# Optimization experiments

Hardware: AMD Instinct MI355X
Metric: run time of the kernel (lower is better)

Reference implementation:

```python
import jax, jax.numpy as jnp
import numpy as np

N_NODES = 500_000
N_EDGES = 5_000_000


def setup_inputs() -> dict:
    key = jax.random.key(0)
    k_x, k_e, k_w1, k_w2 = jax.random.split(key, 4)
    x = jax.random.normal(k_x, (N_NODES, 1), dtype=jnp.float32)
    edge_index = jax.random.randint(k_e, (2, N_EDGES), 0, N_NODES, dtype=jnp.int32)
    # Glorot-style init, matching PyG GCNConv default scale
    W1 = jax.random.normal(k_w1, (1, 16), dtype=jnp.float32) * np.sqrt(2.0 / (1 + 16))
    b1 = jnp.zeros((16,), dtype=jnp.float32)
    W2 = jax.random.normal(k_w2, (16, 1), dtype=jnp.float32) * np.sqrt(2.0 / (16 + 1))
    b2 = jnp.zeros((1,), dtype=jnp.float32)
    return {"x": x, "W1": W1, "b1": b1, "W2": W2, "b2": b2,
            "edge_index": edge_index}


def reference(x, W1, b1, W2, b2, edge_index):
    n = x.shape[0]
    src, dst = edge_index[0], edge_index[1]
    self_idx = jnp.arange(n, dtype=src.dtype)
    # GCNConv default: add self-loops, symmetric normalization deg^-1/2
    src_f = jnp.concatenate([src, self_idx])  # [E+N]
    dst_f = jnp.concatenate([dst, self_idx])  # [E+N]
    deg = jax.ops.segment_sum(jnp.ones(src_f.shape[0], x.dtype), dst_f,
                              num_segments=n)  # [N]
    dinv = jnp.where(deg > 0, jax.lax.rsqrt(jnp.maximum(deg, 1.0)), 0.0)
    norm = dinv[src_f] * dinv[dst_f]  # [E+N] edge weights

    def gcn_conv(h, W, b):
        h = h @ W  # [N, out]
        msg = h[src_f] * norm[:, None]  # gather + scale, [E+N, out]
        agg = jax.ops.segment_sum(msg, dst_f, num_segments=n)  # scatter-add
        return agg + b

    h = jax.nn.relu(gcn_conv(x, W1, b1))  # [N, 16]
    out = gcn_conv(h, W2, b2)  # [N, 1]
    return out.squeeze(-1)  # [N]
```

## Files before the change

### kernel.cpp

```cpp
#include <hip/hip_runtime.h>

#define N_NODES 500000
#define N_EDGES 5000000
#define NB_C 489
#define PB 512
#define EPB 9768
#define SRC_MASK 0xFFFFFu


__global__ __launch_bounds__(1024)
void hist_kernel(const int* __restrict__ dst, unsigned* __restrict__ hist) {
    __shared__ unsigned h[NB_C];
    for (int i = threadIdx.x; i < NB_C; i += 1024) h[i] = 0u;
    __syncthreads();
    const int b = blockIdx.x;
    const long s0 = (long)b * EPB;
    const int n = (int)min((long)EPB, (long)N_EDGES - s0);
    const int4* d4 = (const int4*)(dst + s0);
    const int n4 = n >> 2;
    for (int i = threadIdx.x; i < n4; i += 1024) {
        int4 d = d4[i];
        atomicAdd(&h[d.x >> 10], 1u);
        atomicAdd(&h[d.y >> 10], 1u);
        atomicAdd(&h[d.z >> 10], 1u);
        atomicAdd(&h[d.w >> 10], 1u);
    }
    __syncthreads();
    unsigned* row = hist + (size_t)b * NB_C;
    for (int i = threadIdx.x; i < NB_C; i += 1024) row[i] = h[i];
}

__global__ __launch_bounds__(512)
void prefix_kernel(unsigned* __restrict__ hist, unsigned* __restrict__ binTotal) {
    __shared__ unsigned A[PB], B[PB];
    const int bin = blockIdx.x;
    const int t = threadIdx.x;
    const unsigned c = hist[(size_t)t * NB_C + bin];
    A[t] = c;
    __syncthreads();
    unsigned* cur = A; unsigned* nxt = B;
    for (int off = 1; off < PB; off <<= 1) {
        nxt[t] = cur[t] + (t >= off ? cur[t - off] : 0u);
        __syncthreads();
        unsigned* tmp = cur; cur = nxt; nxt = tmp;
    }
    hist[(size_t)t * NB_C + bin] = cur[t] - c;
    if (t == PB - 1) binTotal[bin] = cur[PB - 1];
}

__global__ __launch_bounds__(512)
void binscan_kernel(const unsigned* __restrict__ binTotal,
                    unsigned* __restrict__ binStart) {
    __shared__ unsigned A[512], B[512];
    const int t = threadIdx.x;
    A[t] = (t < NB_C) ? binTotal[t] : 0u;
    __syncthreads();
    unsigned* cur = A; unsigned* nxt = B;
    for (int off = 1; off < 512; off <<= 1) {
        nxt[t] = cur[t] + (t >= off ? cur[t - off] : 0u);
        __syncthreads();
        unsigned* tmp = cur; cur = nxt; nxt = tmp;
    }
    if (t < NB_C) binStart[t] = (t == 0) ? 0u : cur[t - 1];
    if (t == 0) binStart[NB_C] = cur[NB_C - 1];
}

__global__ __launch_bounds__(1024)
void place_kernel(const int* __restrict__ src, const int* __restrict__ dst,
                  const unsigned* __restrict__ hist,
                  const unsigned* __restrict__ binStart,
                  unsigned* __restrict__ edgebuf) {
    __shared__ unsigned base[NB_C];
    const int b = blockIdx.x;
    const unsigned* row = hist + (size_t)b * NB_C;
    for (int i = threadIdx.x; i < NB_C; i += 1024) base[i] = binStart[i] + row[i];
    __syncthreads();
    const long s0 = (long)b * EPB;
    const int n = (int)min((long)EPB, (long)N_EDGES - s0);
    const int4* s4 = (const int4*)(src + s0);
    const int4* d4 = (const int4*)(dst + s0);
    const int n4 = n >> 2;
    for (int i = threadIdx.x; i < n4; i += 1024) {
        int4 s = s4[i];
        int4 d = d4[i];
        unsigned p;
        p = atomicAdd(&base[d.x >> 10], 1u);
        edgebuf[p] = ((unsigned)(d.x & 1023) << 20) | (unsigned)s.x;
        p = atomicAdd(&base[d.y >> 10], 1u);
        edgebuf[p] = ((unsigned)(d.y & 1023) << 20) | (unsigned)s.y;
        p = atomicAdd(&base[d.z >> 10], 1u);
        edgebuf[p] = ((unsigned)(d.z & 1023) << 20) | (unsigned)s.z;
        p = atomicAdd(&base[d.w >> 10], 1u);
        edgebuf[p] = ((unsigned)(d.w & 1023) << 20) | (unsigned)s.w;
    }
}

__global__ __launch_bounds__(1024)
void deg_dinv_kernel(const unsigned* __restrict__ edgebuf,
                     const unsigned* __restrict__ binStart,
                     const float* __restrict__ x,
                     float* __restrict__ dinv, float* __restrict__ u) {
    __shared__ unsigned cnt[1024];
    cnt[threadIdx.x] = 0u;
    __syncthreads();
    const int bin = blockIdx.x;
    const unsigned e0 = binStart[bin], e1 = binStart[bin + 1];
    const unsigned ea = (e0 + 3u) & ~3u;
    const unsigned eb = e1 & ~3u;
    for (unsigned e = e0 + threadIdx.x; e < min(ea, e1); e += 1024)
        atomicAdd(&cnt[edgebuf[e] >> 20], 1u);
    if (ea < eb) {
        const uint4* p4 = (const uint4*)(edgebuf + ea);
        const unsigned nv = (eb - ea) >> 2;
        for (unsigned i = threadIdx.x; i < nv; i += 1024) {
            uint4 r = p4[i];
            atomicAdd(&cnt[r.x >> 20], 1u);
            atomicAdd(&cnt[r.y >> 20], 1u);
            atomicAdd(&cnt[r.z >> 20], 1u);
            atomicAdd(&cnt[r.w >> 20], 1u);
        }
    }
    for (unsigned e = max(eb, min(ea, e1)) + threadIdx.x; e < e1; e += 1024)
        atomicAdd(&cnt[edgebuf[e] >> 20], 1u);
    __syncthreads();
    const int node = (bin << 10) + threadIdx.x;
    if (node < N_NODES) {
        float di = rsqrtf((float)cnt[threadIdx.x] + 1.0f);
        dinv[node] = di;
        u[node] = x[node] * di;
    }
}

__global__ __launch_bounds__(1024)
void agg1_kernel(const unsigned* __restrict__ edgebuf,
                 const unsigned* __restrict__ binStart,
                 const float* __restrict__ dinv, const float* __restrict__ u,
                 const float* __restrict__ W1, const float* __restrict__ b1,
                 const float* __restrict__ W2, float* __restrict__ w) {
    __shared__ float sum[1024];
    sum[threadIdx.x] = 0.0f;
    __syncthreads();
    const int bin = blockIdx.x;
    const unsigned e0 = binStart[bin], e1 = binStart[bin + 1];
    const unsigned ea = (e0 + 3u) & ~3u;
    const unsigned eb = e1 & ~3u;
    for (unsigned e = e0 + threadIdx.x; e < min(ea, e1); e += 1024) {
        unsigned rec = edgebuf[e];
        atomicAdd(&sum[rec >> 20], u[rec & SRC_MASK]);
    }
    if (ea < eb) {
        const uint4* p4 = (const uint4*)(edgebuf + ea);
        const unsigned nv = (eb - ea) >> 2;
        for (unsigned i = threadIdx.x; i < nv; i += 1024) {
            uint4 r = p4[i];
            atomicAdd(&sum[r.x >> 20], u[r.x & SRC_MASK]);
            atomicAdd(&sum[r.y >> 20], u[r.y & SRC_MASK]);
            atomicAdd(&sum[r.z >> 20], u[r.z & SRC_MASK]);
            atomicAdd(&sum[r.w >> 20], u[r.w & SRC_MASK]);
        }
    }
    for (unsigned e = max(eb, min(ea, e1)) + threadIdx.x; e < e1; e += 1024) {
        unsigned rec = edgebuf[e];
        atomicAdd(&sum[rec >> 20], u[rec & SRC_MASK]);
    }
    __syncthreads();
    const int node = (bin << 10) + threadIdx.x;
    if (node < N_NODES) {
        float di = dinv[node];
        float s = di * (sum[threadIdx.x] + u[node]);
        float t = 0.0f;
#pragma unroll
        for (int j = 0; j < 16; ++j) {
            float h = fmaf(W1[j], s, b1[j]);
            h = fmaxf(h, 0.0f);
            t = fmaf(h, W2[j], t);
        }
        w[node] = t * di;
    }
}

__global__ __launch_bounds__(1024)
void agg2_kernel(const unsigned* __restrict__ edgebuf,
                 const unsigned* __restrict__ binStart,
                 const float* __restrict__ dinv, const float* __restrict__ w,
                 const float* __restrict__ b2, float* __restrict__ out) {
    __shared__ float sum[1024];
    sum[threadIdx.x] = 0.0f;
    __syncthreads();
    const int bin = blockIdx.x;
    const unsigned e0 = binStart[bin], e1 = binStart[bin + 1];
    const unsigned ea = (e0 + 3u) & ~3u;
    const unsigned eb = e1 & ~3u;
    for (unsigned e = e0 + threadIdx.x; e < min(ea, e1); e += 1024) {
        unsigned rec = edgebuf[e];
        atomicAdd(&sum[rec >> 20], w[rec & SRC_MASK]);
    }
    if (ea < eb) {
        const uint4* p4 = (const uint4*)(edgebuf + ea);
        const unsigned nv = (eb - ea) >> 2;
        for (unsigned i = threadIdx.x; i < nv; i += 1024) {
            uint4 r = p4[i];
            atomicAdd(&sum[r.x >> 20], w[r.x & SRC_MASK]);
            atomicAdd(&sum[r.y >> 20], w[r.y & SRC_MASK]);
            atomicAdd(&sum[r.z >> 20], w[r.z & SRC_MASK]);
            atomicAdd(&sum[r.w >> 20], w[r.w & SRC_MASK]);
        }
    }
    for (unsigned e = max(eb, min(ea, e1)) + threadIdx.x; e < e1; e += 1024) {
        unsigned rec = edgebuf[e];
        atomicAdd(&sum[rec >> 20], w[rec & SRC_MASK]);
    }
    __syncthreads();
    const int node = (bin << 10) + threadIdx.x;
    if (node < N_NODES)
        out[node] = fmaf(dinv[node], sum[threadIdx.x] + w[node], b2[0]);
}

__global__ __launch_bounds__(256)
void deg_kernel(const int* __restrict__ dst, float* __restrict__ deg) {
    const int tid = blockIdx.x * blockDim.x + threadIdx.x;
    const int stride = gridDim.x * blockDim.x;
    const int nvec = N_EDGES / 4;
    const int4* dst4 = (const int4*)dst;
    for (int i = tid; i < nvec; i += stride) {
        int4 d = dst4[i];
        atomicAdd(&deg[d.x], 1.0f);
        atomicAdd(&deg[d.y], 1.0f);
        atomicAdd(&deg[d.z], 1.0f);
        atomicAdd(&deg[d.w], 1.0f);
    }
}
__global__ __launch_bounds__(256)
void node1_kernel(const float* __restrict__ x, float* __restrict__ deg_to_dinv,
                  float* __restrict__ u) {
    const int i = blockIdx.x * blockDim.x + threadIdx.x;
    if (i >= N_NODES) return;
    float di = rsqrtf(deg_to_dinv[i] + 1.0f);
    deg_to_dinv[i] = di;
    u[i] = x[i] * di;
}
__global__ __launch_bounds__(256)
void scatter_kernel(const int* __restrict__ src, const int* __restrict__ dst,
                    const float* __restrict__ val, float* __restrict__ acc) {
    const int tid = blockIdx.x * blockDim.x + threadIdx.x;
    const int stride = gridDim.x * blockDim.x;
    const int nvec = N_EDGES / 4;
    const int4* src4 = (const int4*)src;
    const int4* dst4 = (const int4*)dst;
    for (int i = tid; i < nvec; i += stride) {
        int4 s = src4[i];
        int4 d = dst4[i];
        atomicAdd(&acc[d.x], val[s.x]);
        atomicAdd(&acc[d.y], val[s.y]);
        atomicAdd(&acc[d.z], val[s.z]);
        atomicAdd(&acc[d.w], val[s.w]);
    }
}
__global__ __launch_bounds__(256)
void node2_kernel(const float* __restrict__ dinv, const float* __restrict__ u,
                  const float* __restrict__ acc1, const float* __restrict__ W1,
                  const float* __restrict__ b1, const float* __restrict__ W2,
                  float* __restrict__ w) {
    const int i = blockIdx.x * blockDim.x + threadIdx.x;
    if (i >= N_NODES) return;
    float di = dinv[i];
    float s = di * (acc1[i] + u[i]);
    float t = 0.0f;
#pragma unroll
    for (int j = 0; j < 16; ++j) {
        float h = fmaf(W1[j], s, b1[j]);
        h = fmaxf(h, 0.0f);
        t = fmaf(h, W2[j], t);
    }
    w[i] = t * di;
}
__global__ __launch_bounds__(256)
void final_kernel(const float* __restrict__ dinv, const float* __restrict__ w,
                  const float* __restrict__ acc2, const float* __restrict__ b2,
                  float* __restrict__ out) {
    const int i = blockIdx.x * blockDim.x + threadIdx.x;
    if (i >= N_NODES) return;
    float wi = w[i];
    out[i] = fmaf(dinv[i], acc2[i] + wi, b2[0]);
}

extern "C" void kernel_launch(void* const* d_in, const int* in_sizes, int n_in,
                              void* d_out, int out_size, void* d_ws, size_t ws_size,
                              hipStream_t stream) {
    const float* x  = (const float*)d_in[0];
    const float* W1 = (const float*)d_in[1];
    const float* b1 = (const float*)d_in[2];
    const float* W2 = (const float*)d_in[3];
    const float* b2 = (const float*)d_in[4];
    const int* edge_index = (const int*)d_in[5];
    const int* src = edge_index;
    const int* dst = edge_index + N_EDGES;
    float* out = (float*)d_out;
    char* ws = (char*)d_ws;

    const size_t OFF_EDGEBUF  = 0;
    const size_t OFF_HIST     = 20000000;
    const size_t OFF_BINSTART = 21001472;
    const size_t OFF_BINTOTAL = 21003440;
    const size_t OFF_DINV     = 21005408;
    const size_t OFF_U        = OFF_DINV + 2000000;
    const size_t OFF_W        = OFF_U + 2000000;
    const size_t FAST_WS      = OFF_W + 2000000;

    if (ws_size >= FAST_WS) {
        unsigned* edgebuf  = (unsigned*)(ws + OFF_EDGEBUF);
        unsigned* hist     = (unsigned*)(ws + OFF_HIST);
        unsigned* binStart = (unsigned*)(ws + OFF_BINSTART);
        unsigned* binTotal = (unsigned*)(ws + OFF_BINTOTAL);
        float* dinv = (float*)(ws + OFF_DINV);
        float* u    = (float*)(ws + OFF_U);
        float* w    = (float*)(ws + OFF_W);

        hist_kernel<<<PB, 1024, 0, stream>>>(dst, hist);
        prefix_kernel<<<NB_C, PB, 0, stream>>>(hist, binTotal);
        binscan_kernel<<<1, 512, 0, stream>>>(binTotal, binStart);
        place_kernel<<<PB, 1024, 0, stream>>>(src, dst, hist, binStart, edgebuf);
        deg_dinv_kernel<<<NB_C, 1024, 0, stream>>>(edgebuf, binStart, x, dinv, u);
        agg1_kernel<<<NB_C, 1024, 0, stream>>>(edgebuf, binStart, dinv, u, W1, b1, W2, w);
        agg2_kernel<<<NB_C, 1024, 0, stream>>>(edgebuf, binStart, dinv, w, b2, out);
    } else {
        float* buf  = (float*)d_ws;
        float* dinv = buf;
        float* acc1 = buf + 1 * N_NODES;
        float* acc2 = buf + 2 * N_NODES;
        float* u    = buf + 3 * N_NODES;
        float* w    = out;
        hipMemsetAsync(d_ws, 0, 3 * N_NODES * sizeof(float), stream);
        const int nodeBlocks = (N_NODES + 255) / 256;
        const int edgeBlocks = 2048;
        deg_kernel<<<edgeBlocks, 256, 0, stream>>>(dst, dinv);
        node1_kernel<<<nodeBlocks, 256, 0, stream>>>(x, dinv, u);
        scatter_kernel<<<edgeBlocks, 256, 0, stream>>>(src, dst, u, acc1);
        node2_kernel<<<nodeBlocks, 256, 0, stream>>>(dinv, u, acc1, W1, b1, W2, w);
        scatter_kernel<<<edgeBlocks, 256, 0, stream>>>(src, dst, w, acc2);
        final_kernel<<<nodeBlocks, 256, 0, stream>>>(dinv, w, acc2, b2, out);
    }
}
```

Measured before the change: 191.4 us.

## Stage bucketed edges in LDS and write them out coalesced per bin

The place kernel now recounts its chunk's bin histogram in shared memory, scans it, and scatters the packed edge records into a local LDS buffer sorted by bin. Each wave then copies whole bins contiguously to the global edge buffer. This replaces the random global scatter writes with coalesced runs. In exchange it rereads dst, adds a block scan and more barriers, uses about 45KB of LDS, and halves the block size, which may lower occupancy.

After: 181.9 us. -5.0%, faster.

```diff
diff --git a/kernel.cpp b/kernel.cpp
--- a/kernel.cpp
+++ b/kernel.cpp
@@ -65,33 +65,76 @@
     if (t == 0) binStart[NB_C] = cur[NB_C - 1];
 }
 
-__global__ __launch_bounds__(1024)
+__global__ __launch_bounds__(512)
 void place_kernel(const int* __restrict__ src, const int* __restrict__ dst,
                   const unsigned* __restrict__ hist,
                   const unsigned* __restrict__ binStart,
                   unsigned* __restrict__ edgebuf) {
-    __shared__ unsigned base[NB_C];
+    __shared__ unsigned lcnt[NB_C];
+    __shared__ unsigned lstart[NB_C];
+    __shared__ unsigned gbase[NB_C];
+    __shared__ unsigned bump[NB_C];
+    __shared__ unsigned scanA[512], scanB[512];
+    __shared__ unsigned recs[EPB];
+
     const int b = blockIdx.x;
+    const int t = threadIdx.x;
     const unsigned* row = hist + (size_t)b * NB_C;
-    for (int i = threadIdx.x; i < NB_C; i += 1024) base[i] = binStart[i] + row[i];
+    for (int i = t; i < NB_C; i += 512) {
+        lcnt[i] = 0u;
+        bump[i] = 0u;
+        gbase[i] = binStart[i] + row[i];
+    }
     __syncthreads();
     const long s0 = (long)b * EPB;
     const int n = (int)min((long)EPB, (long)N_EDGES - s0);
+    const int4* d4 = (const int4*)(dst + s0);
     const int4* s4 = (const int4*)(src + s0);
-    const int4* d4 = (const int4*)(dst + s0);
     const int n4 = n >> 2;
-    for (int i = threadIdx.x; i < n4; i += 1024) {
+    for (int i = t; i < n4; i += 512) {
+        int4 d = d4[i];
+        atomicAdd(&lcnt[d.x >> 10], 1u);
+        atomicAdd(&lcnt[d.y >> 10], 1u);
+        atomicAdd(&lcnt[d.z >> 10], 1u);
+        atomicAdd(&lcnt[d.w >> 10], 1u);
+    }
+    __syncthreads();
+    scanA[t] = (t < NB_C) ? lcnt[t] : 0u;
+    __syncthreads();
+    unsigned* cur = scanA; unsigned* nxt = scanB;
+    for (int off = 1; off < 512; off <<= 1) {
+        nxt[t] = cur[t] + (t >= off ? cur[t - off] : 0u);
+        __syncthreads();
+        unsigned* tmp = cur; cur = nxt; nxt = tmp;
+    }
+    if (t < NB_C) lstart[t] = cur[t] - lcnt[t];
+    __syncthreads();
+    for (int i = t; i < n4; i += 512) {
         int4 s = s4[i];
         int4 d = d4[i];
-        unsigned p;
-        p = atomicAdd(&base[d.x >> 10], 1u);
-        edgebuf[p] = ((unsigned)(d.x & 1023) << 20) | (unsigned)s.x;
-        p = atomicAdd(&base[d.y >> 10], 1u);
-        edgebuf[p] = ((unsigned)(d.y & 1023) << 20) | (unsigned)s.y;
-        p = atomicAdd(&base[d.z >> 10], 1u);
-        edgebuf[p] = ((unsigned)(d.z & 1023) << 20) | (unsigned)s.z;
-        p = atomicAdd(&base[d.w >> 10], 1u);
-        edgebuf[p] = ((unsigned)(d.w & 1023) << 20) | (unsigned)s.w;
+        unsigned bin, pos;
+        bin = (unsigned)d.x >> 10;
+        pos = lstart[bin] + atomicAdd(&bump[bin], 1u);
+        recs[pos] = ((unsigned)(d.x & 1023) << 20) | (unsigned)s.x;
+        bin = (unsigned)d.y >> 10;
+        pos = lstart[bin] + atomicAdd(&bump[bin], 1u);
+        recs[pos] = ((unsigned)(d.y & 1023) << 20) | (unsigned)s.y;
+        bin = (unsigned)d.z >> 10;
+        pos = lstart[bin] + atomicAdd(&bump[bin], 1u);
+        recs[pos] = ((unsigned)(d.z & 1023) << 20) | (unsigned)s.z;
+        bin = (unsigned)d.w >> 10;
+        pos = lstart[bin] + atomicAdd(&bump[bin], 1u);
+        recs[pos] = ((unsigned)(d.w & 1023) << 20) | (unsigned)s.w;
+    }
+    __syncthreads();
+    const int wave = t >> 6;
+    const int lane = t & 63;
+    for (int bin = wave; bin < NB_C; bin += 8) {
+        const unsigned L  = lcnt[bin];
+        const unsigned gs = gbase[bin];
+        const unsigned ls = lstart[bin];
+        for (unsigned i = lane; i < L; i += 64)
+            edgebuf[gs + i] = recs[ls + i];
     }
 }
 
@@ -319,7 +362,7 @@
         hist_kernel<<<PB, 1024, 0, stream>>>(dst, hist);
         prefix_kernel<<<NB_C, PB, 0, stream>>>(hist, binTotal);
         binscan_kernel<<<1, 512, 0, stream>>>(binTotal, binStart);
-        place_kernel<<<PB, 1024, 0, stream>>>(src, dst, hist, binStart, edgebuf);
+        place_kernel<<<PB, 512, 0, stream>>>(src, dst, hist, binStart, edgebuf);
         deg_dinv_kernel<<<NB_C, 1024, 0, stream>>>(edgebuf, binStart, x, dinv, u);
         agg1_kernel<<<NB_C, 1024, 0, stream>>>(edgebuf, binStart, dinv, u, W1, b1, W2, w);
         agg2_kernel<<<NB_C, 1024, 0, stream>>>(edgebuf, binStart, dinv, w, b2, out);
```
